# Kernel optimization log

Hardware: AMD Instinct MI355X
Metric: run time of the kernel (lower is better)

## Reference

```python
import jax, jax.numpy as jnp
import numpy as np

# ---- GLIFR / network constants (from RSNNNetwork.__init__ with defaults) ----
DT = 0.05
TAU = 5.0
KM = 1.0 / TAU          # k_m = 1/tau
R = 1.0 / 9.43
KSYN = 1.0
SPIKE_R = 20.0
SIGMA_V = 10.0
AVG = 5.0               # scalar mean of `target` (fixed constant here)
THRESH = float(SIGMA_V * np.log((SPIKE_R - AVG) / AVG))
ASC_AMP = np.array([-9.18, -198.94], np.float32)
ASC_R = np.array([1.0, 1.0], np.float32)
ASC_K = np.array([0.003, 0.1], np.float32)
DSDT = 0.9


def _wt(n_post):
    # weight-init center from RSNNNetwork.__init__
    wt = TAU / R * (SIGMA_V / DT) * (DSDT / n_post ** 2)
    wt = wt * (1.0 / (AVG * (1.0 - AVG / SPIKE_R))) / 1000.0
    return float(wt)


def setup_inputs() -> dict:
    key = jax.random.key(0)
    k1, k2, k3 = jax.random.split(key, 3)
    T, B, N0, N1 = 1000, 32, 256, 512
    inputs = jax.random.uniform(k1, (T, B, 1, N0), dtype=jnp.float32)
    wt = _wt(N1)
    W1 = jax.random.uniform(k2, (N1, N0), dtype=jnp.float32, minval=wt - 1.0, maxval=wt + 1.0)
    Wr = jax.random.uniform(k3, (N1, N1), dtype=jnp.float32, minval=wt - 1.0, maxval=wt + 1.0)
    return {"inputs": inputs, "W1": W1, "Wr": Wr}


_AK = jnp.asarray(ASC_K).reshape(2, 1, 1, 1)
_AA = jnp.asarray(ASC_AMP).reshape(2, 1, 1, 1)
_AR = jnp.asarray(ASC_R).reshape(2, 1, 1, 1)


def _glif_step(state, x):
    """Rate-based GLIF (GLIFR) update. state = (V, ascs, Isyn, delay_buf).
    V:[B,1,N], ascs:[2,B,1,N], Isyn:[B,1,N], buf:[delay,B,1,N].
    Returns (new_state, delayed_output, spikes)."""
    V, ascs, Isyn, buf = state
    Isyn = Isyn * (1.0 - DT * KSYN) + DT * KSYN * x          # synaptic current
    V = V * (1.0 - DT * KM) + DT * KM * R * (Isyn + ascs.sum(0))
    S = SPIKE_R * jax.nn.sigmoid((V - THRESH) / SIGMA_V)      # continuous firing rate
    ascs = ascs * (1.0 - DT * _AK) + _AA * _AR * S * DT        # after-spike currents
    out = buf[0]                                               # delay = 1 step
    buf = jnp.concatenate([buf[1:], S[None]], axis=0)
    return (V, ascs, Isyn, buf), out, S


def _zero_state(B, n):
    return (jnp.zeros((B, 1, n), jnp.float32),
            jnp.zeros((2, B, 1, n), jnp.float32),
            jnp.zeros((B, 1, n), jnp.float32),
            jnp.zeros((1, B, 1, n), jnp.float32))


def reference(inputs, W1, Wr):
    T, B = inputs.shape[0], inputs.shape[1]
    N0, N1 = inputs.shape[-1], W1.shape[0]

    def step(carry, x_t):
        s0, s1 = carry
        # input-layer GLIF (no linear)
        s0, o0, _ = _glif_step(s0, x_t)
        # feedforward linear -> glif1 (first call this step)
        h1 = jnp.einsum('bin,mn->bim', o0, W1)
        s1, o1, sp_a = _glif_step(s1, h1)
        # recurrent linear -> SAME glif1 again (second call this step)
        h2 = jnp.einsum('bin,mn->bim', o1, Wr)
        s1, _, sp_b = _glif_step(s1, h2)
        return (s0, s1), jnp.stack([sp_a, sp_b], axis=0)

    init = (_zero_state(B, N0), _zero_state(B, N1))
    _, spikes = jax.lax.scan(step, init, inputs)  # [T, 2, B, 1, N1]
    # spikes_all of the last GLIF: two appends per timestep, interleaved in call order
    return spikes.reshape(T * 2, B, 1, N1)
```

## Files before the change

### kernel.cpp

```cpp
#include <hip/hip_runtime.h>


#define T_STEPS 1000
#define NB 32
#define N0 256
#define N1 512

#define C_SYN_D 0.95f
#define C_SYN_I 0.05f
#define C_V_D   0.99f
#define C_KMR   0.0010604453870625663f
#define C_TH    10.986122886681098f
#define C_A0_D  0.99985f
#define C_A0_I  (-0.459f)
#define C_A1_D  0.995f
#define C_A1_I  (-9.947f)

__device__ __forceinline__ float glif_S(float V) {
  return 20.0f / (1.0f + __expf((C_TH - V) * 0.1f));
}

__global__ __launch_bounds__(64)
void layer0_scan(const float* __restrict__ x, float* __restrict__ S0) {
  const int g = blockIdx.x * 64 + threadIdx.x;
  float V = 0.f, a0 = 0.f, a1 = 0.f, Is = 0.f;
  float xb[8];
#pragma unroll
  for (int i = 0; i < 8; ++i) xb[i] = x[i * (NB * N0) + g];
#pragma unroll 1
  for (int tb = 0; tb < T_STEPS / 8; ++tb) {
#pragma unroll
    for (int u = 0; u < 8; ++u) {
      const int t = tb * 8 + u;
      const float xi = xb[u];
      const int tf = t + 8;
      if (tf < T_STEPS) xb[u] = x[tf * (NB * N0) + g];
      Is = fmaf(Is, C_SYN_D, C_SYN_I * xi);
      V  = fmaf(V, C_V_D, C_KMR * (Is + a0 + a1));
      const float S = glif_S(V);
      a0 = fmaf(a0, C_A0_D, C_A0_I * S);
      a1 = fmaf(a1, C_A1_D, C_A1_I * S);
      S0[t * (NB * N0) + g] = S;
    }
  }
}

__global__ __launch_bounds__(256, 1)
void rsnn_recur(const float* __restrict__ W1, const float* __restrict__ Wr,
                const float* __restrict__ S0, float* __restrict__ out,
                unsigned* __restrict__ bar) {
  const int wg  = blockIdx.x;
  const int b   = wg >> 3;
  const int s   = wg & 7;
  const int tid = threadIdx.x;
  const int mg  = tid >> 4;
  const int kc  = tid & 15;
  const int mBase = s * 64 + mg * 4;

  __shared__ float actS[16 * 36];
  __shared__ float actO[16 * 20];

  float4 wr4[4][8];
  float4 w14[4][4];
#pragma unroll
  for (int i = 0; i < 4; ++i) {
    const float4* rw = (const float4*)(Wr + (size_t)(mBase + i) * N1 + kc * 32);
#pragma unroll
    for (int j = 0; j < 8; ++j) wr4[i][j] = rw[j];
    const float4* r1 = (const float4*)(W1 + (size_t)(mBase + i) * N0 + kc * 16);
#pragma unroll
    for (int j = 0; j < 4; ++j) w14[i][j] = r1[j];
  }

  float V[4]   = {0.f, 0.f, 0.f, 0.f};
  float A0v[4] = {0.f, 0.f, 0.f, 0.f};
  float A1v[4] = {0.f, 0.f, 0.f, 0.f};
  float Is[4]  = {0.f, 0.f, 0.f, 0.f};
  unsigned* cnt = bar + b * 32;

#pragma unroll 1
  for (int t = 0; t < T_STEPS; ++t) {
    if (t == 0) {
      actS[(tid >> 5) * 36 + (tid & 31)] = 0.f;
      {
        const int k = tid + 256;
        actS[(k >> 5) * 36 + (k & 31)] = 0.f;
      }
      actO[(tid >> 4) * 20 + (tid & 15)] = 0.f;
    } else {
      const float* pS = out + ((size_t)(2 * t - 1) * NB + b) * N1;
      const float v0 = __hip_atomic_load(pS + tid,       __ATOMIC_RELAXED, __HIP_MEMORY_SCOPE_AGENT);
      const float v1 = __hip_atomic_load(pS + tid + 256, __ATOMIC_RELAXED, __HIP_MEMORY_SCOPE_AGENT);
      const float v2 = S0[(size_t)(t - 1) * (NB * N0) + b * N0 + tid];
      actS[(tid >> 5) * 36 + (tid & 31)] = v0;
      {
        const int k = tid + 256;
        actS[(k >> 5) * 36 + (k & 31)] = v1;
      }
      actO[(tid >> 4) * 20 + (tid & 15)] = v2;
    }
    __syncthreads();

    float h2a[4] = {0.f, 0.f, 0.f, 0.f};
    float h1a[4] = {0.f, 0.f, 0.f, 0.f};
    const float4* aS4 = (const float4*)actS;
    const float4* aO4 = (const float4*)actO;
#pragma unroll
    for (int j = 0; j < 8; ++j) {
      const float4 a = aS4[kc * 9 + j];
#pragma unroll
      for (int i = 0; i < 4; ++i) {
        h2a[i] = fmaf(wr4[i][j].x, a.x, h2a[i]);
        h2a[i] = fmaf(wr4[i][j].y, a.y, h2a[i]);
        h2a[i] = fmaf(wr4[i][j].z, a.z, h2a[i]);
        h2a[i] = fmaf(wr4[i][j].w, a.w, h2a[i]);
      }
    }
#pragma unroll
    for (int j = 0; j < 4; ++j) {
      const float4 a = aO4[kc * 5 + j];
#pragma unroll
      for (int i = 0; i < 4; ++i) {
        h1a[i] = fmaf(w14[i][j].x, a.x, h1a[i]);
        h1a[i] = fmaf(w14[i][j].y, a.y, h1a[i]);
        h1a[i] = fmaf(w14[i][j].z, a.z, h1a[i]);
        h1a[i] = fmaf(w14[i][j].w, a.w, h1a[i]);
      }
    }

#pragma unroll
    for (int mask = 1; mask <= 8; mask <<= 1) {
#pragma unroll
      for (int i = 0; i < 4; ++i) {
        h2a[i] += __shfl_xor(h2a[i], mask, 64);
        h1a[i] += __shfl_xor(h1a[i], mask, 64);
      }
    }

    if (kc == 0) {
      float spa[4], spb[4];
#pragma unroll
      for (int i = 0; i < 4; ++i) {
        Is[i] = fmaf(Is[i], C_SYN_D, C_SYN_I * h1a[i]);
        V[i]  = fmaf(V[i], C_V_D, C_KMR * (Is[i] + A0v[i] + A1v[i]));
        const float Sa = glif_S(V[i]);
        A0v[i] = fmaf(A0v[i], C_A0_D, C_A0_I * Sa);
        A1v[i] = fmaf(A1v[i], C_A1_D, C_A1_I * Sa);
        spa[i] = Sa;
        Is[i] = fmaf(Is[i], C_SYN_D, C_SYN_I * h2a[i]);
        V[i]  = fmaf(V[i], C_V_D, C_KMR * (Is[i] + A0v[i] + A1v[i]));
        const float Sb = glif_S(V[i]);
        A0v[i] = fmaf(A0v[i], C_A0_D, C_A0_I * Sb);
        A1v[i] = fmaf(A1v[i], C_A1_D, C_A1_I * Sb);
        spb[i] = Sb;
      }
      float* outA = out + ((size_t)(2 * t) * NB + b) * N1 + mBase;
      *(float4*)outA = make_float4(spa[0], spa[1], spa[2], spa[3]);
      float* outB = out + ((size_t)(2 * t + 1) * NB + b) * N1 + mBase;
#pragma unroll
      for (int i = 0; i < 4; ++i)
        __hip_atomic_store(outB + i, spb[i], __ATOMIC_RELAXED, __HIP_MEMORY_SCOPE_AGENT);
    }

    if (t < T_STEPS - 1) {
      __syncthreads();
      if (tid == 0) {
        __hip_atomic_fetch_add(cnt, 1u, __ATOMIC_RELAXED, __HIP_MEMORY_SCOPE_AGENT);
        const unsigned tgt = 8u * (unsigned)(t + 1);
        while (__hip_atomic_load(cnt, __ATOMIC_RELAXED, __HIP_MEMORY_SCOPE_AGENT) < tgt) {}
      }
      __syncthreads();
    }
  }
}

extern "C" void kernel_launch(void* const* d_in, const int* in_sizes, int n_in,
                              void* d_out, int out_size, void* d_ws, size_t ws_size,
                              hipStream_t stream) {
  const float* inputs = (const float*)d_in[0];
  const float* W1     = (const float*)d_in[1];
  const float* Wr     = (const float*)d_in[2];
  float* out = (float*)d_out;

  float* S0 = (float*)d_ws;
  unsigned* bar = (unsigned*)((char*)d_ws +
                              (size_t)T_STEPS * NB * N0 * sizeof(float));

  hipMemsetAsync(bar, 0, NB * 32 * sizeof(unsigned), stream);

  hipLaunchKernelGGL(layer0_scan, dim3((NB * N0) / 64), dim3(64), 0, stream,
                     inputs, S0);

  void* args[5];
  args[0] = (void*)&W1;
  args[1] = (void*)&Wr;
  args[2] = (void*)&S0;
  args[3] = (void*)&out;
  args[4] = (void*)&bar;
  hipLaunchCooperativeKernel((const void*)rsnn_recur, dim3(256), dim3(256),
                             args, 0, stream);
}
```

Measured before the change: 2.828 ms.

## Overlap feedforward GLIF update with recurrent barrier wait and remap workgroups

Each step is split so the feedforward matvec and first GLIF update run before waiting on the per-batch barrier. The wait now sits only in front of the recurrent matvec, and arrival is signalled right after the recurrent spikes are written, which hides part of the barrier latency behind independent work. Workgroups for one batch are spread across the grid instead of being adjacent, and the recurrent spike stores are packed into two 64-bit atomic stores. The relaxed atomics are not paired with acquire/release fences, so the code depends on store visibility ordering.

```diff
diff --git a/kernel.cpp b/kernel.cpp
--- a/kernel.cpp
+++ b/kernel.cpp
@@ -50,8 +50,8 @@
                 const float* __restrict__ S0, float* __restrict__ out,
                 unsigned* __restrict__ bar) {
   const int wg  = blockIdx.x;
-  const int b   = wg >> 3;
-  const int s   = wg & 7;
+  const int b   = wg & 31;
+  const int s   = wg >> 5;
   const int tid = threadIdx.x;
   const int mg  = tid >> 4;
   const int kc  = tid & 15;
@@ -80,42 +80,15 @@
 
 #pragma unroll 1
   for (int t = 0; t < T_STEPS; ++t) {
-    if (t == 0) {
-      actS[(tid >> 5) * 36 + (tid & 31)] = 0.f;
-      {
-        const int k = tid + 256;
-        actS[(k >> 5) * 36 + (k & 31)] = 0.f;
-      }
-      actO[(tid >> 4) * 20 + (tid & 15)] = 0.f;
-    } else {
-      const float* pS = out + ((size_t)(2 * t - 1) * NB + b) * N1;
-      const float v0 = __hip_atomic_load(pS + tid,       __ATOMIC_RELAXED, __HIP_MEMORY_SCOPE_AGENT);
-      const float v1 = __hip_atomic_load(pS + tid + 256, __ATOMIC_RELAXED, __HIP_MEMORY_SCOPE_AGENT);
-      const float v2 = S0[(size_t)(t - 1) * (NB * N0) + b * N0 + tid];
-      actS[(tid >> 5) * 36 + (tid & 31)] = v0;
-      {
-        const int k = tid + 256;
-        actS[(k >> 5) * 36 + (k & 31)] = v1;
-      }
+    {
+      const float v2 = (t == 0) ? 0.f
+                     : S0[(size_t)(t - 1) * (NB * N0) + b * N0 + tid];
       actO[(tid >> 4) * 20 + (tid & 15)] = v2;
     }
     __syncthreads();
 
-    float h2a[4] = {0.f, 0.f, 0.f, 0.f};
     float h1a[4] = {0.f, 0.f, 0.f, 0.f};
-    const float4* aS4 = (const float4*)actS;
     const float4* aO4 = (const float4*)actO;
-#pragma unroll
-    for (int j = 0; j < 8; ++j) {
-      const float4 a = aS4[kc * 9 + j];
-#pragma unroll
-      for (int i = 0; i < 4; ++i) {
-        h2a[i] = fmaf(wr4[i][j].x, a.x, h2a[i]);
-        h2a[i] = fmaf(wr4[i][j].y, a.y, h2a[i]);
-        h2a[i] = fmaf(wr4[i][j].z, a.z, h2a[i]);
-        h2a[i] = fmaf(wr4[i][j].w, a.w, h2a[i]);
-      }
-    }
 #pragma unroll
     for (int j = 0; j < 4; ++j) {
       const float4 a = aO4[kc * 5 + j];
@@ -127,18 +100,13 @@
         h1a[i] = fmaf(w14[i][j].w, a.w, h1a[i]);
       }
     }
-
 #pragma unroll
     for (int mask = 1; mask <= 8; mask <<= 1) {
 #pragma unroll
-      for (int i = 0; i < 4; ++i) {
-        h2a[i] += __shfl_xor(h2a[i], mask, 64);
-        h1a[i] += __shfl_xor(h1a[i], mask, 64);
-      }
-    }
-
+      for (int i = 0; i < 4; ++i) h1a[i] += __shfl_xor(h1a[i], mask, 64);
+    }
     if (kc == 0) {
-      float spa[4], spb[4];
+      float spa[4];
 #pragma unroll
       for (int i = 0; i < 4; ++i) {
         Is[i] = fmaf(Is[i], C_SYN_D, C_SYN_I * h1a[i]);
@@ -147,6 +115,56 @@
         A0v[i] = fmaf(A0v[i], C_A0_D, C_A0_I * Sa);
         A1v[i] = fmaf(A1v[i], C_A1_D, C_A1_I * Sa);
         spa[i] = Sa;
+      }
+      float* outA = out + ((size_t)(2 * t) * NB + b) * N1 + mBase;
+      *(float4*)outA = make_float4(spa[0], spa[1], spa[2], spa[3]);
+    }
+
+    if (t > 0) {
+      if (tid == 0) {
+        const unsigned tgt = 8u * (unsigned)t;
+        while (__hip_atomic_load(cnt, __ATOMIC_RELAXED, __HIP_MEMORY_SCOPE_AGENT) < tgt) {}
+      }
+    }
+    __syncthreads();
+
+    {
+      float v0, v1;
+      if (t == 0) {
+        v0 = v1 = 0.f;
+      } else {
+        const float* pS = out + ((size_t)(2 * t - 1) * NB + b) * N1;
+        v0 = __hip_atomic_load(pS + tid,       __ATOMIC_RELAXED, __HIP_MEMORY_SCOPE_AGENT);
+        v1 = __hip_atomic_load(pS + tid + 256, __ATOMIC_RELAXED, __HIP_MEMORY_SCOPE_AGENT);
+      }
+      actS[(tid >> 5) * 36 + (tid & 31)] = v0;
+      const int k = tid + 256;
+      actS[(k >> 5) * 36 + (k & 31)] = v1;
+    }
+    __syncthreads();
+
+    float h2a[4] = {0.f, 0.f, 0.f, 0.f};
+    const float4* aS4 = (const float4*)actS;
+#pragma unroll
+    for (int j = 0; j < 8; ++j) {
+      const float4 a = aS4[kc * 9 + j];
+#pragma unroll
+      for (int i = 0; i < 4; ++i) {
+        h2a[i] = fmaf(wr4[i][j].x, a.x, h2a[i]);
+        h2a[i] = fmaf(wr4[i][j].y, a.y, h2a[i]);
+        h2a[i] = fmaf(wr4[i][j].z, a.z, h2a[i]);
+        h2a[i] = fmaf(wr4[i][j].w, a.w, h2a[i]);
+      }
+    }
+#pragma unroll
+    for (int mask = 1; mask <= 8; mask <<= 1) {
+#pragma unroll
+      for (int i = 0; i < 4; ++i) h2a[i] += __shfl_xor(h2a[i], mask, 64);
+    }
+    if (kc == 0) {
+      float spb[4];
+#pragma unroll
+      for (int i = 0; i < 4; ++i) {
         Is[i] = fmaf(Is[i], C_SYN_D, C_SYN_I * h2a[i]);
         V[i]  = fmaf(V[i], C_V_D, C_KMR * (Is[i] + A0v[i] + A1v[i]));
         const float Sb = glif_S(V[i]);
@@ -154,22 +172,20 @@
         A1v[i] = fmaf(A1v[i], C_A1_D, C_A1_I * Sb);
         spb[i] = Sb;
       }
-      float* outA = out + ((size_t)(2 * t) * NB + b) * N1 + mBase;
-      *(float4*)outA = make_float4(spa[0], spa[1], spa[2], spa[3]);
       float* outB = out + ((size_t)(2 * t + 1) * NB + b) * N1 + mBase;
-#pragma unroll
-      for (int i = 0; i < 4; ++i)
-        __hip_atomic_store(outB + i, spb[i], __ATOMIC_RELAXED, __HIP_MEMORY_SCOPE_AGENT);
-    }
-
-    if (t < T_STEPS - 1) {
-      __syncthreads();
-      if (tid == 0) {
-        __hip_atomic_fetch_add(cnt, 1u, __ATOMIC_RELAXED, __HIP_MEMORY_SCOPE_AGENT);
-        const unsigned tgt = 8u * (unsigned)(t + 1);
-        while (__hip_atomic_load(cnt, __ATOMIC_RELAXED, __HIP_MEMORY_SCOPE_AGENT) < tgt) {}
-      }
-      __syncthreads();
+      const unsigned long long q0 =
+          ((unsigned long long)__float_as_uint(spb[1]) << 32) | __float_as_uint(spb[0]);
+      const unsigned long long q1 =
+          ((unsigned long long)__float_as_uint(spb[3]) << 32) | __float_as_uint(spb[2]);
+      __hip_atomic_store((unsigned long long*)outB,       q0,
+                         __ATOMIC_RELAXED, __HIP_MEMORY_SCOPE_AGENT);
+      __hip_atomic_store((unsigned long long*)(outB + 2), q1,
+                         __ATOMIC_RELAXED, __HIP_MEMORY_SCOPE_AGENT);
+    }
+
+    __syncthreads();
+    if (tid == 0) {
+      __hip_atomic_fetch_add(cnt, 1u, __ATOMIC_RELAXED, __HIP_MEMORY_SCOPE_AGENT);
     }
   }
 }
```

Result: slower. 2.894 ms (+2.4%).
